# Optimization experiments

Measured on AMD Instinct MI355X. Metric: run time of the kernel, lower is better.

Reference implementation:

```python
import jax, jax.numpy as jnp
import numpy as np

B, L, D, K = 8, 1024, 1024, 128
VOCAB, N_ATOM_FEAT, N_TIMESTEPS = 160, 512, 1000
NEG = jnp.finfo(jnp.float32).min
SCALING = K ** (-0.5)


def setup_inputs() -> dict:
    key = jax.random.key(0)
    ks = jax.random.split(key, 14)
    inp = {}
    # forward args
    inp["token_id"] = jax.random.randint(ks[0], (B, L), 0, VOCAB)  # 0 => padding
    inp["node_attr"] = jax.random.randint(ks[1], (B, L, 9), 0, N_ATOM_FEAT)
    inp["is_molecule"] = jax.random.randint(ks[2], (B,), 0, 2).astype(bool)
    inp["pos"] = jax.random.normal(ks[3], (B, L, 3), jnp.float32) * 10.0
    inp["time_step"] = jax.random.randint(ks[4], (B, L), 0, N_TIMESTEPS)
    # learned parameters
    inp["embed_table"] = jax.random.normal(ks[5], (VOCAB, D), jnp.float32) * 0.02
    inp["atom_feat_table"] = jax.random.normal(ks[6], (N_ATOM_FEAT, D), jnp.float32) * 0.02
    inp["time_table"] = jax.random.normal(ks[7], (N_TIMESTEPS, D), jnp.float32) * 0.02
    inp["time_w1"] = jax.random.normal(ks[8], (D, D), jnp.float32) * (D ** -0.5)
    inp["time_b1"] = jnp.zeros((D,), jnp.float32)
    inp["time_w2"] = jax.random.normal(ks[9], (D, D), jnp.float32) * (D ** -0.5)
    inp["time_b2"] = jnp.zeros((D,), jnp.float32)
    inp["pos_emb_w"] = jax.random.normal(ks[10], (1, K), jnp.float32)          # Linear(1 -> K), no bias
    inp["pos_feature_w"] = jax.random.normal(ks[11], (K, D), jnp.float32) * (K ** -0.5)  # Linear(K -> D), no bias
    return inp


def _pos_emb(pos, padding_mask, pos_emb_w, pos_feature_w):
    # pos: [B,L,3], padding_mask: [B,L] bool
    delta = pos[:, :, None, :] - pos[:, None, :, :]          # [B,L,L,3]
    dist = 1.0 / (jnp.linalg.norm(delta, axis=-1) + 1.0)     # [B,L,L]
    # masked_fill on key side (expand_mask) and query side (padding_mask)
    mask = padding_mask[:, None, :] | padding_mask[:, :, None]
    dist = jnp.where(mask, NEG, dist)
    # value projection: Linear(1->K) on per-atom radial norm, zeroed at padding
    pe = jnp.linalg.norm(pos, axis=-1, keepdims=True) @ pos_emb_w  # [B,L,K]
    pe = jnp.where(padding_mask[:, :, None], 0.0, pe)
    attn = jax.nn.softmax(dist * SCALING, axis=-1)            # [B,L,L]
    pfe = jnp.einsum("bqk,bkc->bqc", attn, pe)                 # [B,L,K]
    pfe = pfe @ pos_feature_w                                  # [B,L,D]
    return jnp.where(padding_mask[:, :, None], 0.0, pfe)


def reference(token_id, node_attr, is_molecule, pos, time_step,
              embed_table, atom_feat_table, time_table,
              time_w1, time_b1, time_w2, time_b2,
              pos_emb_w, pos_feature_w):
    padding_mask = token_id == 0                               # [B,L]
    x = embed_table[token_id]                                  # [B,L,D]
    # 2D atom features: embed cols 1: and sum over feature axis
    atom_emb = atom_feat_table[node_attr[:, :, 1:]].sum(axis=-2)  # [B,L,D]
    atom_emb = jnp.where(is_molecule[:, None, None], atom_emb, 0.0)
    x = x + atom_emb
    # time step encoder: learnable embedding + Linear-SiLU-Linear MLP
    t = time_table[time_step]                                   # [B,L,D]
    time_embed = jax.nn.silu(t @ time_w1 + time_b1) @ time_w2 + time_b2
    x = x + time_embed
    # pairwise 3D positional embedding (softmax attention over 1/(r+1))
    x = x + _pos_emb(pos, padding_mask, pos_emb_w, pos_feature_w)
    return x, padding_mask
```

## Files before the change

kernel.cpp:

```cpp
#include <hip/hip_runtime.h>
#include <hip/hip_bf16.h>
#include <math.h>

#define BB 8
#define LL 1024
#define DD 1024
#define KK 128
#define NTS 1000
#define SCALE 0.08838834764831845f

typedef __attribute__((ext_vector_type(8))) short short8;
typedef __attribute__((ext_vector_type(4))) float f32x4;

__device__ __forceinline__ unsigned short f2bf(float x) {
    __hip_bfloat16 h = __float2bfloat16(x);
    return *reinterpret_cast<unsigned short*>(&h);
}

__global__ __launch_bounds__(256) void prep_kernel(
    const float* __restrict__ time_table,
    const float* __restrict__ w1,
    const float* __restrict__ w2,
    const float* __restrict__ pos_emb_w,
    const float* __restrict__ pos_feature_w,
    const void*  __restrict__ is_mol_raw,
    unsigned short* __restrict__ Tbf,
    unsigned short* __restrict__ W1t,
    unsigned short* __restrict__ W2t,
    float* __restrict__ v,
    int*   __restrict__ is_mol_out)
{
    __shared__ float tile[32][33];
    const int blk = blockIdx.x;

    if (blk < 1024) {
        int e = (blk * 256 + threadIdx.x) * 4;
        ushort4 o;
        if (e < NTS * DD) {
            float4 vv = *(const float4*)&time_table[e];
            o.x = f2bf(vv.x); o.y = f2bf(vv.y); o.z = f2bf(vv.z); o.w = f2bf(vv.w);
        } else {
            o.x = o.y = o.z = o.w = 0;
        }
        *(ushort4*)&Tbf[e] = o;
    } else if (blk < 3072) {
        const int which = (blk - 1024) >> 10;
        const int idx = (blk - 1024) & 1023;
        const float* in = which ? w2 : w1;
        unsigned short* out = which ? W2t : W1t;
        const int bx = (idx & 31) * 32, by = (idx >> 5) * 32;
        const int tx = threadIdx.x & 31, ty = threadIdx.x >> 5;
        #pragma unroll
        for (int r = 0; r < 32; r += 8)
            tile[ty + r][tx] = in[(size_t)(by + ty + r) * DD + bx + tx];
        __syncthreads();
        #pragma unroll
        for (int r = 0; r < 32; r += 8)
            out[(size_t)(bx + ty + r) * DD + by + tx] = f2bf(tile[tx][ty + r]);
    } else if (blk < 3076) {
        int d = (blk - 3072) * 256 + threadIdx.x;
        float acc = 0.0f;
        #pragma unroll 4
        for (int c = 0; c < KK; ++c)
            acc += pos_emb_w[c] * pos_feature_w[c * DD + d];
        v[d] = acc;
    } else {
        if (threadIdx.x == 0) {
            const int* ip = (const int*)is_mol_raw;
            const unsigned char* cp = (const unsigned char*)is_mol_raw;
            bool all_bin = true;
            for (int i = 0; i < BB; ++i) {
                int x = ip[i];
                if (x != 0 && x != 1) all_bin = false;
            }
            for (int i = 0; i < BB; ++i)
                is_mol_out[i] = all_bin ? (ip[i] != 0) : (cp[i] != 0);
        }
    }
}

template <int MODE>
__global__ __launch_bounds__(256) void mfma_gemm(
    const unsigned short* __restrict__ A,
    const unsigned short* __restrict__ Bt,
    const float* __restrict__ bias,
    void* __restrict__ Cout)
{
    __shared__ __align__(16) unsigned short As[64][72];
    __shared__ __align__(16) unsigned short Bs[64][72];

    const int tid  = threadIdx.x;
    const int lane = tid & 63;
    const int wave = tid >> 6;
    const int wm = wave >> 1, wn = wave & 1;
    const int quad = lane >> 4, l16 = lane & 15;
    const int mBase = blockIdx.y * 64, nBase = blockIdx.x * 64;

    f32x4 acc[2][2] = {{{0.f,0.f,0.f,0.f},{0.f,0.f,0.f,0.f}},
                       {{0.f,0.f,0.f,0.f},{0.f,0.f,0.f,0.f}}};

    const int r0 = tid >> 3,         ko0 = (tid & 7) << 3;
    const int r1 = (tid + 256) >> 3, ko1 = ko0;

    for (int k0 = 0; k0 < DD; k0 += 64) {
        float4 a0 = *(const float4*)&A [(size_t)(mBase + r0) * DD + k0 + ko0];
        float4 a1 = *(const float4*)&A [(size_t)(mBase + r1) * DD + k0 + ko1];
        float4 b0 = *(const float4*)&Bt[(size_t)(nBase + r0) * DD + k0 + ko0];
        float4 b1 = *(const float4*)&Bt[(size_t)(nBase + r1) * DD + k0 + ko1];
        *(float4*)&As[r0][ko0] = a0;
        *(float4*)&As[r1][ko1] = a1;
        *(float4*)&Bs[r0][ko0] = b0;
        *(float4*)&Bs[r1][ko1] = b1;
        __syncthreads();

        #pragma unroll
        for (int kk = 0; kk < 64; kk += 32) {
            short8 af0 = *(const short8*)&As[wm * 32 +      l16][kk + quad * 8];
            short8 af1 = *(const short8*)&As[wm * 32 + 16 + l16][kk + quad * 8];
            short8 bf0 = *(const short8*)&Bs[wn * 32 +      l16][kk + quad * 8];
            short8 bf1 = *(const short8*)&Bs[wn * 32 + 16 + l16][kk + quad * 8];
            acc[0][0] = __builtin_amdgcn_mfma_f32_16x16x32_bf16(af0, bf0, acc[0][0], 0, 0, 0);
            acc[0][1] = __builtin_amdgcn_mfma_f32_16x16x32_bf16(af0, bf1, acc[0][1], 0, 0, 0);
            acc[1][0] = __builtin_amdgcn_mfma_f32_16x16x32_bf16(af1, bf0, acc[1][0], 0, 0, 0);
            acc[1][1] = __builtin_amdgcn_mfma_f32_16x16x32_bf16(af1, bf1, acc[1][1], 0, 0, 0);
        }
        __syncthreads();
    }

    #pragma unroll
    for (int mi = 0; mi < 2; ++mi) {
        #pragma unroll
        for (int ni = 0; ni < 2; ++ni) {
            const int col = nBase + wn * 32 + ni * 16 + l16;
            const float bv = bias[col];
            #pragma unroll
            for (int r = 0; r < 4; ++r) {
                const int row = mBase + wm * 32 + mi * 16 + quad * 4 + r;
                float val = acc[mi][ni][r] + bv;
                if (MODE == 0) {
                    val = val / (1.0f + expf(-val));
                    ((unsigned short*)Cout)[(size_t)row * DD + col] = f2bf(val);
                } else {
                    ((float*)Cout)[(size_t)row * DD + col] = val;
                }
            }
        }
    }
}

__global__ __launch_bounds__(256) void fused_all(
    const int*   __restrict__ token_id,
    const int*   __restrict__ node_attr,
    const float* __restrict__ pos,
    const int*   __restrict__ time_step,
    const float* __restrict__ embed_table,
    const float* __restrict__ atom_feat_table,
    const float* __restrict__ E,
    const float* __restrict__ v,
    const int*   __restrict__ is_mol,
    float* __restrict__ out)
{
    __shared__ float4 keys[LL];
    __shared__ float  sS[8];

    const int blk   = blockIdx.x;
    const int batch = blk >> 7;
    const int q0    = (blk & 127) << 3;
    const int tid   = threadIdx.x;
    const int lane  = tid & 63, wave = tid >> 6;

    #pragma unroll
    for (int i = 0; i < 4; ++i) {
        const int k = tid + i * 256;
        const int t = batch * LL + k;
        const float x = pos[t * 3 + 0];
        const float y = pos[t * 3 + 1];
        const float z = pos[t * 3 + 2];
        const int tok = token_id[t];
        const float n = sqrtf(x * x + y * y + z * z);
        keys[k] = make_float4(x, y, z, tok == 0 ? -1.0f : n);
    }
    __syncthreads();

    #pragma unroll
    for (int qi = 0; qi < 2; ++qi) {
        const int ql = wave * 2 + qi;
        const float4 qk = keys[q0 + ql];
        float lsum = 0.0f, lws = 0.0f;
        #pragma unroll 4
        for (int i = 0; i < 16; ++i) {
            const float4 kd = keys[lane + i * 64];
            const float dx = qk.x - kd.x, dy = qk.y - kd.y, dz = qk.z - kd.z;
            const float dn = sqrtf(dx * dx + dy * dy + dz * dz);
            const float e = __expf(SCALE / (dn + 1.0f));
            const bool valid = kd.w >= 0.0f;
            const float ev = valid ? e : 0.0f;
            lsum += ev;
            lws  += ev * (valid ? kd.w : 0.0f);
        }
        #pragma unroll
        for (int off = 32; off > 0; off >>= 1) {
            lsum += __shfl_xor(lsum, off);
            lws  += __shfl_xor(lws,  off);
        }
        if (lane == 0)
            sS[ql] = (qk.w < 0.0f) ? 0.0f : (lws / lsum);
    }
    __syncthreads();

    const int im = is_mol[batch];
    const int j  = tid * 4;
    const float4 vv = *(const float4*)&v[j];

    for (int ql = 0; ql < 8; ++ql) {
        const int t   = batch * LL + q0 + ql;
        const int tok = token_id[t];
        const int ts  = time_step[t];
        const float s = sS[ql];

        float4 acc = *(const float4*)&embed_table[(size_t)tok * DD + j];
        if (im) {
            #pragma unroll
            for (int f = 1; f < 9; ++f) {
                const int a = node_attr[t * 9 + f];
                const float4 av = *(const float4*)&atom_feat_table[(size_t)a * DD + j];
                acc.x += av.x; acc.y += av.y; acc.z += av.z; acc.w += av.w;
            }
        }
        const float4 ev = *(const float4*)&E[(size_t)ts * DD + j];
        acc.x += ev.x + s * vv.x;
        acc.y += ev.y + s * vv.y;
        acc.z += ev.z + s * vv.z;
        acc.w += ev.w + s * vv.w;
        *(float4*)&out[(size_t)t * DD + j] = acc;
    }

    if (tid < 8) {
        const int t = batch * LL + q0 + tid;
        out[(size_t)BB * LL * DD + t] = (keys[q0 + tid].w < 0.0f) ? 1.0f : 0.0f;
    }
}

extern "C" void kernel_launch(void* const* d_in, const int* in_sizes, int n_in,
                              void* d_out, int out_size, void* d_ws, size_t ws_size,
                              hipStream_t stream)
{
    const int*   token_id      = (const int*)  d_in[0];
    const int*   node_attr     = (const int*)  d_in[1];
    const void*  is_mol_raw    = (const void*) d_in[2];
    const float* pos           = (const float*)d_in[3];
    const int*   time_step     = (const int*)  d_in[4];
    const float* embed_table   = (const float*)d_in[5];
    const float* atom_feat     = (const float*)d_in[6];
    const float* time_table    = (const float*)d_in[7];
    const float* w1            = (const float*)d_in[8];
    const float* b1            = (const float*)d_in[9];
    const float* w2            = (const float*)d_in[10];
    const float* b2            = (const float*)d_in[11];
    const float* pos_emb_w     = (const float*)d_in[12];
    const float* pos_feature_w = (const float*)d_in[13];

    float* out = (float*)d_out;
    float* Wf  = (float*)d_ws;

    unsigned short* Tbf = (unsigned short*)Wf;
    unsigned short* W1t = (unsigned short*)(Wf + 524288);
    float*          E   = Wf;
    unsigned short* H   = (unsigned short*)(Wf + 1048576);
    unsigned short* W2t = (unsigned short*)(Wf + 1048576 + 524288);
    float* V     = Wf + 2097152;
    int*   is_mol_res = (int*)(V + 1024);

    prep_kernel<<<3077, 256, 0, stream>>>(time_table, w1, w2, pos_emb_w,
                                          pos_feature_w, is_mol_raw,
                                          Tbf, W1t, W2t, V, is_mol_res);

    dim3 g(16, 16);
    mfma_gemm<0><<<g, 256, 0, stream>>>(Tbf, W1t, b1, (void*)H);
    mfma_gemm<1><<<g, 256, 0, stream>>>(H, W2t, b2, (void*)E);

    fused_all<<<1024, 256, 0, stream>>>(token_id, node_attr, pos, time_step,
                                        embed_table, atom_feat, E, V,
                                        is_mol_res, out);
}
```

Baseline: 158.6 us.

## Store gather tables in bf16, fuse time-table conversion into GEMM, shrink GEMM tiles

```diff
diff --git a/kernel.cpp b/kernel.cpp
--- a/kernel.cpp
+++ b/kernel.cpp
@@ -7,6 +7,8 @@
 #define DD 1024
 #define KK 128
 #define NTS 1000
+#define VOCAB 160
+#define NATOM 512
 #define SCALE 0.08838834764831845f
 
 typedef __attribute__((ext_vector_type(8))) short short8;
@@ -16,36 +18,31 @@
     __hip_bfloat16 h = __float2bfloat16(x);
     return *reinterpret_cast<unsigned short*>(&h);
 }
+__device__ __forceinline__ float bf2f(unsigned short u) {
+    return __uint_as_float(((unsigned int)u) << 16);
+}
 
 __global__ __launch_bounds__(256) void prep_kernel(
-    const float* __restrict__ time_table,
     const float* __restrict__ w1,
     const float* __restrict__ w2,
+    const float* __restrict__ embed_f,
+    const float* __restrict__ atom_f,
     const float* __restrict__ pos_emb_w,
     const float* __restrict__ pos_feature_w,
     const void*  __restrict__ is_mol_raw,
-    unsigned short* __restrict__ Tbf,
     unsigned short* __restrict__ W1t,
     unsigned short* __restrict__ W2t,
+    unsigned short* __restrict__ embed_bf,
+    unsigned short* __restrict__ atom_bf,
     float* __restrict__ v,
     int*   __restrict__ is_mol_out)
 {
     __shared__ float tile[32][33];
     const int blk = blockIdx.x;
 
-    if (blk < 1024) {
-        int e = (blk * 256 + threadIdx.x) * 4;
-        ushort4 o;
-        if (e < NTS * DD) {
-            float4 vv = *(const float4*)&time_table[e];
-            o.x = f2bf(vv.x); o.y = f2bf(vv.y); o.z = f2bf(vv.z); o.w = f2bf(vv.w);
-        } else {
-            o.x = o.y = o.z = o.w = 0;
-        }
-        *(ushort4*)&Tbf[e] = o;
-    } else if (blk < 3072) {
-        const int which = (blk - 1024) >> 10;
-        const int idx = (blk - 1024) & 1023;
+    if (blk < 2048) {
+        const int which = blk >> 10;
+        const int idx = blk & 1023;
         const float* in = which ? w2 : w1;
         unsigned short* out = which ? W2t : W1t;
         const int bx = (idx & 31) * 32, by = (idx >> 5) * 32;
@@ -57,8 +54,18 @@
         #pragma unroll
         for (int r = 0; r < 32; r += 8)
             out[(size_t)(bx + ty + r) * DD + by + tx] = f2bf(tile[tx][ty + r]);
-    } else if (blk < 3076) {
-        int d = (blk - 3072) * 256 + threadIdx.x;
+    } else if (blk < 2208) {
+        const int e = ((blk - 2048) * 256 + threadIdx.x) * 4;
+        float4 vv = *(const float4*)&embed_f[e];
+        ushort4 o = { f2bf(vv.x), f2bf(vv.y), f2bf(vv.z), f2bf(vv.w) };
+        *(ushort4*)&embed_bf[e] = o;
+    } else if (blk < 2720) {
+        const int e = ((blk - 2208) * 256 + threadIdx.x) * 4;
+        float4 vv = *(const float4*)&atom_f[e];
+        ushort4 o = { f2bf(vv.x), f2bf(vv.y), f2bf(vv.z), f2bf(vv.w) };
+        *(ushort4*)&atom_bf[e] = o;
+    } else if (blk < 2724) {
+        int d = (blk - 2720) * 256 + threadIdx.x;
         float acc = 0.0f;
         #pragma unroll 4
         for (int c = 0; c < KK; ++c)
@@ -80,71 +87,62 @@
 }
 
 template <int MODE>
-__global__ __launch_bounds__(256) void mfma_gemm(
-    const unsigned short* __restrict__ A,
+__global__ __launch_bounds__(256) void mfma_gemm32(
+    const void* __restrict__ Ap,
     const unsigned short* __restrict__ Bt,
     const float* __restrict__ bias,
-    void* __restrict__ Cout)
+    unsigned short* __restrict__ Cout)
 {
-    __shared__ __align__(16) unsigned short As[64][72];
-    __shared__ __align__(16) unsigned short Bs[64][72];
+    __shared__ __align__(16) unsigned short As[32][72];
+    __shared__ __align__(16) unsigned short Bs[32][72];
 
     const int tid  = threadIdx.x;
     const int lane = tid & 63;
     const int wave = tid >> 6;
     const int wm = wave >> 1, wn = wave & 1;
     const int quad = lane >> 4, l16 = lane & 15;
-    const int mBase = blockIdx.y * 64, nBase = blockIdx.x * 64;
-
-    f32x4 acc[2][2] = {{{0.f,0.f,0.f,0.f},{0.f,0.f,0.f,0.f}},
-                       {{0.f,0.f,0.f,0.f},{0.f,0.f,0.f,0.f}}};
-
-    const int r0 = tid >> 3,         ko0 = (tid & 7) << 3;
-    const int r1 = (tid + 256) >> 3, ko1 = ko0;
+    const int mBase = blockIdx.y * 32, nBase = blockIdx.x * 32;
+
+    f32x4 acc = {0.f, 0.f, 0.f, 0.f};
+
+    const int r = tid >> 3, ko = (tid & 7) * 8;
+    const int rowB = nBase + r;
+    int rowA = mBase + r;
+    if (MODE == 0 && rowA >= NTS) rowA = NTS - 1;
 
     for (int k0 = 0; k0 < DD; k0 += 64) {
-        float4 a0 = *(const float4*)&A [(size_t)(mBase + r0) * DD + k0 + ko0];
-        float4 a1 = *(const float4*)&A [(size_t)(mBase + r1) * DD + k0 + ko1];
-        float4 b0 = *(const float4*)&Bt[(size_t)(nBase + r0) * DD + k0 + ko0];
-        float4 b1 = *(const float4*)&Bt[(size_t)(nBase + r1) * DD + k0 + ko1];
-        *(float4*)&As[r0][ko0] = a0;
-        *(float4*)&As[r1][ko1] = a1;
-        *(float4*)&Bs[r0][ko0] = b0;
-        *(float4*)&Bs[r1][ko1] = b1;
+        if (MODE == 0) {
+            const float* A = (const float*)Ap;
+            float4 a0 = *(const float4*)&A[(size_t)rowA * DD + k0 + ko];
+            float4 a1 = *(const float4*)&A[(size_t)rowA * DD + k0 + ko + 4];
+            short8 s8;
+            s8[0] = f2bf(a0.x); s8[1] = f2bf(a0.y); s8[2] = f2bf(a0.z); s8[3] = f2bf(a0.w);
+            s8[4] = f2bf(a1.x); s8[5] = f2bf(a1.y); s8[6] = f2bf(a1.z); s8[7] = f2bf(a1.w);
+            *(short8*)&As[r][ko] = s8;
+        } else {
+            const unsigned short* A = (const unsigned short*)Ap;
+            *(float4*)&As[r][ko] = *(const float4*)&A[(size_t)rowA * DD + k0 + ko];
+        }
+        *(float4*)&Bs[r][ko] = *(const float4*)&Bt[(size_t)rowB * DD + k0 + ko];
         __syncthreads();
 
         #pragma unroll
         for (int kk = 0; kk < 64; kk += 32) {
-            short8 af0 = *(const short8*)&As[wm * 32 +      l16][kk + quad * 8];
-            short8 af1 = *(const short8*)&As[wm * 32 + 16 + l16][kk + quad * 8];
-            short8 bf0 = *(const short8*)&Bs[wn * 32 +      l16][kk + quad * 8];
-            short8 bf1 = *(const short8*)&Bs[wn * 32 + 16 + l16][kk + quad * 8];
-            acc[0][0] = __builtin_amdgcn_mfma_f32_16x16x32_bf16(af0, bf0, acc[0][0], 0, 0, 0);
-            acc[0][1] = __builtin_amdgcn_mfma_f32_16x16x32_bf16(af0, bf1, acc[0][1], 0, 0, 0);
-            acc[1][0] = __builtin_amdgcn_mfma_f32_16x16x32_bf16(af1, bf0, acc[1][0], 0, 0, 0);
-            acc[1][1] = __builtin_amdgcn_mfma_f32_16x16x32_bf16(af1, bf1, acc[1][1], 0, 0, 0);
+            short8 af = *(const short8*)&As[wm * 16 + l16][kk + quad * 8];
+            short8 bf = *(const short8*)&Bs[wn * 16 + l16][kk + quad * 8];
+            acc = __builtin_amdgcn_mfma_f32_16x16x32_bf16(af, bf, acc, 0, 0, 0);
         }
         __syncthreads();
     }
 
+    const int col = nBase + wn * 16 + l16;
+    const float bv = bias[col];
     #pragma unroll
-    for (int mi = 0; mi < 2; ++mi) {
-        #pragma unroll
-        for (int ni = 0; ni < 2; ++ni) {
-            const int col = nBase + wn * 32 + ni * 16 + l16;
-            const float bv = bias[col];
-            #pragma unroll
-            for (int r = 0; r < 4; ++r) {
-                const int row = mBase + wm * 32 + mi * 16 + quad * 4 + r;
-                float val = acc[mi][ni][r] + bv;
-                if (MODE == 0) {
-                    val = val / (1.0f + expf(-val));
-                    ((unsigned short*)Cout)[(size_t)row * DD + col] = f2bf(val);
-                } else {
-                    ((float*)Cout)[(size_t)row * DD + col] = val;
-                }
-            }
-        }
+    for (int r4 = 0; r4 < 4; ++r4) {
+        const int row = mBase + wm * 16 + quad * 4 + r4;
+        float val = acc[r4] + bv;
+        if (MODE == 0) val = val / (1.0f + __expf(-val));
+        Cout[(size_t)row * DD + col] = f2bf(val);
     }
 }
 
@@ -153,9 +151,9 @@
     const int*   __restrict__ node_attr,
     const float* __restrict__ pos,
     const int*   __restrict__ time_step,
-    const float* __restrict__ embed_table,
-    const float* __restrict__ atom_feat_table,
-    const float* __restrict__ E,
+    const unsigned short* __restrict__ embed_bf,
+    const unsigned short* __restrict__ atom_bf,
+    const unsigned short* __restrict__ Ebf,
     const float* __restrict__ v,
     const int*   __restrict__ is_mol,
     float* __restrict__ out)
@@ -208,31 +206,46 @@
     }
     __syncthreads();
 
-    const int im = is_mol[batch];
-    const int j  = tid * 4;
-    const float4 vv = *(const float4*)&v[j];
-
-    for (int ql = 0; ql < 8; ++ql) {
+    const int im   = is_mol[batch];
+    const int half = tid >> 7;
+    const int tl   = tid & 127;
+    const int j    = tl * 8;
+    const float4 v0 = *(const float4*)&v[j];
+    const float4 v1 = *(const float4*)&v[j + 4];
+
+    #pragma unroll
+    for (int qp = 0; qp < 4; ++qp) {
+        const int ql  = qp * 2 + half;
         const int t   = batch * LL + q0 + ql;
         const int tok = token_id[t];
         const int ts  = time_step[t];
         const float s = sS[ql];
 
-        float4 acc = *(const float4*)&embed_table[(size_t)tok * DD + j];
+        float o[8];
+        short8 eb = *(const short8*)&embed_bf[(size_t)tok * DD + j];
+        #pragma unroll
+        for (int d = 0; d < 8; ++d) o[d] = bf2f((unsigned short)eb[d]);
+
         if (im) {
             #pragma unroll
             for (int f = 1; f < 9; ++f) {
                 const int a = node_attr[t * 9 + f];
-                const float4 av = *(const float4*)&atom_feat_table[(size_t)a * DD + j];
-                acc.x += av.x; acc.y += av.y; acc.z += av.z; acc.w += av.w;
+                short8 ab = *(const short8*)&atom_bf[(size_t)a * DD + j];
+                #pragma unroll
+                for (int d = 0; d < 8; ++d) o[d] += bf2f((unsigned short)ab[d]);
             }
         }
-        const float4 ev = *(const float4*)&E[(size_t)ts * DD + j];
-        acc.x += ev.x + s * vv.x;
-        acc.y += ev.y + s * vv.y;
-        acc.z += ev.z + s * vv.z;
-        acc.w += ev.w + s * vv.w;
-        *(float4*)&out[(size_t)t * DD + j] = acc;
+        short8 er = *(const short8*)&Ebf[(size_t)ts * DD + j];
+        #pragma unroll
+        for (int d = 0; d < 8; ++d) o[d] += bf2f((unsigned short)er[d]);
+
+        o[0] += s * v0.x; o[1] += s * v0.y; o[2] += s * v0.z; o[3] += s * v0.w;
+        o[4] += s * v1.x; o[5] += s * v1.y; o[6] += s * v1.z; o[7] += s * v1.w;
+
+        float4 w0 = {o[0], o[1], o[2], o[3]};
+        float4 w1 = {o[4], o[5], o[6], o[7]};
+        *(float4*)&out[(size_t)t * DD + j]     = w0;
+        *(float4*)&out[(size_t)t * DD + j + 4] = w1;
     }
 
     if (tid < 8) {
@@ -261,25 +274,27 @@
     const float* pos_feature_w = (const float*)d_in[13];
 
     float* out = (float*)d_out;
-    float* Wf  = (float*)d_ws;
-
-    unsigned short* Tbf = (unsigned short*)Wf;
-    unsigned short* W1t = (unsigned short*)(Wf + 524288);
-    float*          E   = Wf;
-    unsigned short* H   = (unsigned short*)(Wf + 1048576);
-    unsigned short* W2t = (unsigned short*)(Wf + 1048576 + 524288);
-    float* V     = Wf + 2097152;
-    int*   is_mol_res = (int*)(V + 1024);
-
-    prep_kernel<<<3077, 256, 0, stream>>>(time_table, w1, w2, pos_emb_w,
-                                          pos_feature_w, is_mol_raw,
-                                          Tbf, W1t, W2t, V, is_mol_res);
-
-    dim3 g(16, 16);
-    mfma_gemm<0><<<g, 256, 0, stream>>>(Tbf, W1t, b1, (void*)H);
-    mfma_gemm<1><<<g, 256, 0, stream>>>(H, W2t, b2, (void*)E);
+    char*  ws  = (char*)d_ws;
+
+    unsigned short* W1t      = (unsigned short*)(ws);
+    unsigned short* Ebf      = (unsigned short*)(ws);
+    unsigned short* H        = (unsigned short*)(ws + (2u << 20));
+    unsigned short* W2t      = (unsigned short*)(ws + (4u << 20));
+    unsigned short* embed_bf = (unsigned short*)(ws + (6u << 20));
+    unsigned short* atom_bf  = (unsigned short*)(ws + (6u << 20) + (512u << 10));
+    float*          V        = (float*)(ws + (7u << 20) + (512u << 10));
+    int*            is_mol_r = (int*)(V + 1024);
+
+    prep_kernel<<<2725, 256, 0, stream>>>(w1, w2, embed_table, atom_feat,
+                                          pos_emb_w, pos_feature_w, is_mol_raw,
+                                          W1t, W2t, embed_bf, atom_bf,
+                                          V, is_mol_r);
+
+    dim3 g(32, 32);
+    mfma_gemm32<0><<<g, 256, 0, stream>>>((const void*)time_table, W1t, b1, H);
+    mfma_gemm32<1><<<g, 256, 0, stream>>>((const void*)H,          W2t, b2, Ebf);
 
     fused_all<<<1024, 256, 0, stream>>>(token_id, node_attr, pos, time_step,
-                                        embed_table, atom_feat, E, V,
-                                        is_mol_res, out);
-}
+                                        embed_bf, atom_bf, Ebf, V,
+                                        is_mol_r, out);
+}
```

Measured after the change: 151.7 us. -4.3%, faster.
